# Optimization experiments

Hardware: AMD Instinct MI355X
Metric: run time of the kernel (lower is better)

Reference implementation:

```python
import jax, jax.numpy as jnp
import numpy as np
from jax import lax

B, C, D, H, W = 2, 256, 32, 64, 192
TRAIN_W = 640
DISPS = np.arange(D, dtype=np.float32) * 0.01  # norm_disp_range


def conv1x1(x, w, b):
    # x [B,Cin,H,W], w [Cout,Cin]
    return jnp.einsum('bchw,oc->bohw', x, w) + b[None, :, None, None]


def conv3x3(x, w, b):
    y = lax.conv_general_dilated(x, w, (1, 1), 'SAME',
                                 dimension_numbers=('NCHW', 'OIHW', 'NCHW'))
    return y + b[None, :, None, None]


def warp_volume(x, shift_px):
    """Horizontal bilinear warp with border clamp for each disparity.
    x [B,Cc,H,W], shift_px [B,D] (pixel shift) -> [B,Cc,D,H,W]."""
    Wd = x.shape[3]
    j = jnp.arange(Wd, dtype=x.dtype)
    src = jnp.clip(j[None, None, :] + shift_px[:, :, None], 0.0, Wd - 1.0)  # [B,D,W]
    x0 = jnp.floor(src).astype(jnp.int32)
    x1 = jnp.minimum(x0 + 1, Wd - 1)
    frac = src - x0.astype(src.dtype)  # [B,D,W]

    def one(xb, i0, i1, fb):
        g0 = xb[:, :, i0]  # [Cc,H,D,W]
        g1 = xb[:, :, i1]
        out = g0 * (1.0 - fb) + g1 * fb
        return out.transpose(0, 2, 1, 3)  # [Cc,D,H,W]

    return jax.vmap(one)(x, x0, x1, frac)


def setup_inputs() -> dict:
    key = jax.random.key(0)
    ks = jax.random.split(key, 16)
    f32 = jnp.float32
    inp = {
        't_feat': jax.random.normal(ks[0], (B, C, H, W), f32),
        's_feat': jax.random.normal(ks[1], (B, C, H, W), f32),
        'directs': jnp.ones((B, 1, 1, 1), f32),
        'qw': jax.random.normal(ks[2], (C // 4, C), f32) * 0.05,
        'qb': jax.random.normal(ks[3], (C // 4,), f32) * 0.05,
        'kw': jax.random.normal(ks[4], (C // 4, C), f32) * 0.05,
        'kb': jax.random.normal(ks[5], (C // 4,), f32) * 0.05,
        'vw': jax.random.normal(ks[6], (C // 4, C), f32) * 0.05,
        'vb': jax.random.normal(ks[7], (C // 4,), f32) * 0.05,
        'p1w': jax.random.normal(ks[8], (C // 4, C // 2, 3, 3), f32) * 0.05,
        'p1b': jax.random.normal(ks[9], (C // 4,), f32) * 0.05,
        'p2w': jax.random.normal(ks[10], (D, C // 4, 3, 3), f32) * 0.05,
        'p2b': jax.random.normal(ks[11], (D,), f32) * 0.05,
        'rw': jax.random.normal(ks[12], (C, C + D), f32) * 0.05,
        'rb': jax.random.normal(ks[13], (C,), f32) * 0.05,
        'img_w': TRAIN_W,
    }
    return inp


def reference(t_feat, s_feat, directs, qw, qb, kw, kb, vw, vb,
              p1w, p1b, p2w, p2b, rw, rb, img_w):
    rel_scale = (TRAIN_W / img_w) if img_w != TRAIN_W else 1.0
    q = conv1x1(t_feat, qw, qb)  # [B,C/4,H,W]
    k = conv1x1(s_feat, kw, kb)
    v = conv1x1(s_feat, vw, vb)

    Wd = t_feat.shape[3]
    disps = jnp.asarray(DISPS, t_feat.dtype)
    # normalized shift d*2*rel_scale*directs -> pixels: * (W-1)/2
    shift = disps[None, :] * rel_scale * directs.reshape(-1, 1) * (Wd - 1)  # [B,D]

    wk = warp_volume(k, shift)  # [B,C/4,D,H,W]
    wv = warp_volume(v, shift)

    cq = q.shape[1]
    cost = jnp.einsum('bchw,bcdhw->bdhw', q, wk) / (cq ** 0.5)  # [B,D,H,W]
    norm_cost = jax.nn.softmax(cost, axis=1)
    agg_v = jnp.einsum('bdhw,bcdhw->bchw', norm_cost, wv)  # [B,C/4,H,W]

    h1 = jax.nn.elu(conv3x3(jnp.concatenate([q, agg_v], axis=1), p1w, p1b))
    res_cost = conv3x3(h1, p2w, p2b)  # [B,D,H,W]
    cost = (cost + res_cost) * 0.5
    norm_cost = jax.nn.softmax(cost, axis=1)
    x = jax.nn.elu(conv1x1(jnp.concatenate([t_feat, norm_cost], axis=1), rw, rb))
    return x, cost
```

## Files before the change

kernel.cpp:

```cpp
#include <hip/hip_runtime.h>

#define BB 2
#define CC 256
#define CQ 64
#define DD 32
#define HH 64
#define WW 192
#define HW (HH*WW)
#define NPIX (BB*HW)

typedef __attribute__((ext_vector_type(8))) short bf16x8;
typedef __attribute__((ext_vector_type(4))) float f32x4;

__device__ __forceinline__ float b2f(ushort s){ return __uint_as_float(((uint)s)<<16); }
__device__ __forceinline__ ushort f2b(float f){
    uint u = __float_as_uint(f);
    return (ushort)((u + 0x7fffu + ((u>>16)&1u)) >> 16);
}
__device__ __forceinline__ float eluf(float v){ return v > 0.f ? v : (__expf(v)-1.f); }

__global__ __launch_bounds__(256) void k_prep_feat(
    const float* __restrict__ t_feat, const float* __restrict__ s_feat,
    ushort* __restrict__ Tt, ushort* __restrict__ Ts)
{
    __shared__ ushort sT[64*264];
    int blk = blockIdx.x;
    int which = blk / 384;
    int rem   = blk % 384;
    int b     = rem / 192;
    int tile  = rem % 192;
    int p0    = tile*64;
    const float* src = which ? s_feat : t_feat;
    ushort* dst      = which ? Ts : Tt;
    int tid = threadIdx.x;

    for (int i = tid; i < 2048; i += 256){
        int px  = i & 63;
        int c16 = i >> 6;
        const float* p = src + ((size_t)(b*CC + c16*8))*HW + p0 + px;
        uint u[4];
        #pragma unroll
        for (int j2=0;j2<4;++j2)
            u[j2] = (uint)f2b(p[(size_t)(2*j2)*HW]) | ((uint)f2b(p[(size_t)(2*j2+1)*HW])<<16);
        uint4 q4; q4.x=u[0]; q4.y=u[1]; q4.z=u[2]; q4.w=u[3];
        *(uint4*)&sT[(px*33 + c16)*8] = q4;
    }
    __syncthreads();
    for (int i = tid; i < 2048; i += 256){
        int c16 = i & 31;
        int px  = i >> 5;
        uint4 v = *(const uint4*)&sT[(px*33 + c16)*8];
        *(uint4*)(dst + ((size_t)(b*HW + p0 + px))*CC + c16*8) = v;
    }
}

__global__ __launch_bounds__(256) void k_prep_w(
    const float* __restrict__ qw, const float* __restrict__ qb,
    const float* __restrict__ kw, const float* __restrict__ kb,
    const float* __restrict__ vw, const float* __restrict__ vb,
    const float* __restrict__ p1w, const float* __restrict__ p2w,
    const float* __restrict__ rw,
    ushort* __restrict__ Wqkv, float* __restrict__ bqkv,
    ushort* __restrict__ A1, ushort* __restrict__ A2, ushort* __restrict__ Ar)
{
    int id = blockIdx.x*256 + threadIdx.x;
    if (id < 49152) {
        int o = id / 256, c = id % 256;
        float v = (o<64)? qw[o*256+c] : (o<128)? kw[(o-64)*256+c] : vw[(o-128)*256+c];
        Wqkv[id] = f2b(v);
    } else if (id < 49344) {
        int o = id - 49152;
        bqkv[o] = (o<64)? qb[o] : (o<128)? kb[o-64] : vb[o-128];
    } else if (id < 49344+73728) {
        int i = id - 49344;
        int o = i/1152, r = i%1152, t = r/128, ci = r%128;
        A1[i] = f2b(p1w[(size_t)(o*128+ci)*9 + t]);
    } else if (id < 49344+73728+18432) {
        int i = id - (49344+73728);
        int o = i/576, r = i%576, t = r/64, ci = r%64;
        A2[i] = f2b(p2w[(size_t)(o*64+ci)*9 + t]);
    } else if (id < 49344+73728+18432+73728) {
        int i = id - (49344+73728+18432);
        Ar[i] = f2b(rw[i]);
    }
}

__global__ __launch_bounds__(256) void g_qkv(
    const ushort* __restrict__ Tt, const ushort* __restrict__ Ts,
    const ushort* __restrict__ Wqkv, const float* __restrict__ bqkv,
    ushort* __restrict__ X1, ushort* __restrict__ VbT)
{
    __shared__ ushort sT[32*264];
    __shared__ ushort sS[32*264];
    int tid = threadIdx.x;
    int bid = blockIdx.x;
    int tile = (bid & 7)*96 + (bid >> 3);
    int p0 = tile * 32;

    for (int i = tid; i < 1024; i += 256){
        int px = i >> 5, c16 = i & 31;
        size_t gsrc = ((size_t)(p0 + px))*CC + c16*8;
        *(uint4*)&sT[(px*33 + c16)*8] = *(const uint4*)(Tt + gsrc);
        *(uint4*)&sS[(px*33 + c16)*8] = *(const uint4*)(Ts + gsrc);
    }
    __syncthreads();

    int wv = tid >> 6, lane = tid & 63;
    int lm = lane & 15, lk = lane >> 4;
    f32x4 acc[3][2];
    #pragma unroll
    for (int g=0;g<3;++g){ acc[g][0]=(f32x4){0.f,0.f,0.f,0.f}; acc[g][1]=(f32x4){0.f,0.f,0.f,0.f}; }
    const ushort* Ap = Wqkv + (size_t)(wv*16 + lm)*CC + lk*8;

    #pragma unroll
    for (int k0=0; k0<CC; k0+=32){
        bf16x8 a0 = *(const bf16x8*)(Ap + k0);
        bf16x8 a1 = *(const bf16x8*)(Ap + 64*CC + k0);
        bf16x8 a2 = *(const bf16x8*)(Ap + 128*CC + k0);
        #pragma unroll
        for (int nt=0; nt<2; ++nt){
            int ch = (nt*16+lm)*33 + (k0>>3) + lk;
            bf16x8 bT = *(const bf16x8*)&sT[ch*8];
            bf16x8 bS = *(const bf16x8*)&sS[ch*8];
            acc[0][nt] = __builtin_amdgcn_mfma_f32_16x16x32_bf16(a0, bT, acc[0][nt], 0,0,0);
            acc[1][nt] = __builtin_amdgcn_mfma_f32_16x16x32_bf16(a1, bS, acc[1][nt], 0,0,0);
            acc[2][nt] = __builtin_amdgcn_mfma_f32_16x16x32_bf16(a2, bS, acc[2][nt], 0,0,0);
        }
    }
    int ol = wv*16 + lk*4;
    #pragma unroll
    for (int nt=0; nt<2; ++nt){
        int p = p0 + nt*16 + lm;
        {
            int ob = ol;
            uint u0 = (uint)f2b(acc[0][nt][0]+bqkv[ob])   | ((uint)f2b(acc[0][nt][1]+bqkv[ob+1])<<16);
            uint u1 = (uint)f2b(acc[0][nt][2]+bqkv[ob+2]) | ((uint)f2b(acc[0][nt][3]+bqkv[ob+3])<<16);
            *(uint2*)(X1 + (size_t)p*128 + ol) = make_uint2(u0, u1);
        }
        {
            int ob = 64 + ol;
            uint u0 = (uint)f2b(acc[1][nt][0]+bqkv[ob])   | ((uint)f2b(acc[1][nt][1]+bqkv[ob+1])<<16);
            uint u1 = (uint)f2b(acc[1][nt][2]+bqkv[ob+2]) | ((uint)f2b(acc[1][nt][3]+bqkv[ob+3])<<16);
            *(uint2*)(X1 + (size_t)p*128 + 64 + ol) = make_uint2(u0, u1);
        }
        #pragma unroll
        for (int j=0;j<4;++j)
            VbT[(size_t)(ol+j)*NPIX + p] = f2b(acc[2][nt][j] + bqkv[128 + ol + j]);
    }
}

#define BAND 160
#define VTS 168
#define STS 36
#define PFS 164
__global__ __launch_bounds__(512) void k_ca(
    const ushort* __restrict__ X1, const ushort* __restrict__ VbT,
    const float* __restrict__ directs, const int* __restrict__ img_w_p,
    float* __restrict__ C1, ushort* __restrict__ Agg)
{
    __shared__ ushort sQ[32*64];
    __shared__ ushort sK[BAND*64];
    __shared__ ushort sVT[64*VTS];
    __shared__ float  sF[BAND*STS];
    __shared__ ushort sPC[32*VTS];
    int tid = threadIdx.x;
    int j   = blockIdx.x;
    int r8  = j & 7;
    int kk  = j >> 3;
    int sub = kk % 6;
    int rhi = kk / 6;
    int row = rhi*8 + r8;
    int b   = row >> 6;
    int h   = row & 63;
    int w0  = sub * 32;
    size_t rowbase = (size_t)b*HW + (size_t)h*WW;

    for (int i = tid; i < BAND*8; i += 512){
        int x = i >> 3, c8 = i & 7;
        int gx = w0 - 64 + x;
        uint4 kv = make_uint4(0,0,0,0);
        if (gx >= 0 && gx < WW)
            kv = *(const uint4*)(X1 + (rowbase+gx)*128 + 64 + c8*8);
        *(uint4*)&sK[(x*8 + (c8 ^ (x&7)))*8] = kv;
    }
    for (int i = tid; i < 64*20; i += 512){
        int c = i / 20, k2 = i % 20;
        int gx = w0 - 64 + k2*8;
        uint4 vv = make_uint4(0,0,0,0);
        if (gx >= 0 && gx < WW)
            vv = *(const uint4*)(VbT + (size_t)c*NPIX + rowbase + gx);
        *(uint4*)&sVT[c*VTS + k2*8] = vv;
    }
    if (tid < 256){
        int px = tid >> 3, c8 = tid & 7;
        uint4 qv = *(const uint4*)(X1 + (rowbase + w0 + px)*128 + c8*8);
        *(uint4*)&sQ[(px*8 + (c8 ^ (px&7)))*8] = qv;
    }
    __syncthreads();

    int w8 = tid >> 6, lane = tid & 63;
    int lm = lane & 15, lk = lane >> 4;

    {
        int mt = w8 & 1;
        int qrow = mt*16 + lm;
        for (int nt = (w8 >> 1); nt < 10; nt += 4){
            int xrow = nt*16 + lm;
            f32x4 acc = {0.f,0.f,0.f,0.f};
            #pragma unroll
            for (int kt=0; kt<2; ++kt){
                bf16x8 a = *(const bf16x8*)&sQ[(qrow*8 + ((kt*4+lk) ^ (qrow&7)))*8];
                bf16x8 bbf = *(const bf16x8*)&sK[(xrow*8 + ((kt*4+lk) ^ (xrow&7)))*8];
                acc = __builtin_amdgcn_mfma_f32_16x16x32_bf16(a, bbf, acc, 0,0,0);
            }
            *(f32x4*)&sF[xrow*STS + mt*16 + lk*4] = acc;
        }
    }
    __syncthreads();

    int px  = tid >> 4;
    int l16 = tid & 15;
    int w   = w0 + px;
    size_t n = rowbase + w;
    int imw = img_w_p[0];
    float rel = (imw != 640) ? (640.0f/(float)imw) : 1.0f;
    float sf = 0.01f * rel * directs[b] * 191.0f;
    float wf = (float)w;

    float cost[2]; int xi0[2], xi1[2]; float frk[2];
    #pragma unroll
    for (int t=0; t<2; ++t){
        int d = l16*2 + t;
        float srcx = fminf(fmaxf(wf + (float)d*sf, 0.f), 191.0f);
        int x0 = (int)floorf(srcx);
        int x1 = min(x0+1, WW-1);
        float fr = srcx - (float)x0;
        int i0 = x0 - w0 + 64;
        int i1 = x1 - w0 + 64;
        xi0[t] = i0; xi1[t] = i1; frk[t] = fr;
        float s0 = sF[i0*STS + px];
        float s1 = sF[i1*STS + px];
        cost[t] = (s0 + fr*(s1-s0)) * 0.125f;
    }
    *(float2*)(C1 + n*DD + l16*2) = make_float2(cost[0], cost[1]);
    float mm = fmaxf(cost[0], cost[1]);
    mm = fmaxf(mm, __shfl_xor(mm, 1));
    mm = fmaxf(mm, __shfl_xor(mm, 2));
    mm = fmaxf(mm, __shfl_xor(mm, 4));
    mm = fmaxf(mm, __shfl_xor(mm, 8));
    float e0 = __expf(cost[0]-mm), e1 = __expf(cost[1]-mm);
    float ss = e0 + e1;
    ss += __shfl_xor(ss, 1);
    ss += __shfl_xor(ss, 2);
    ss += __shfl_xor(ss, 4);
    ss += __shfl_xor(ss, 8);
    float inv = 1.f/ss;
    float p0 = e0*inv, p1 = e1*inv;
    __syncthreads();

    for (int i = tid; i < (32*PFS)/4; i += 512)
        *(f32x4*)&sF[i*4] = (f32x4){0.f,0.f,0.f,0.f};
    __syncthreads();

    {
        float w1a = p0*frk[0], w0a = p0 - w1a;
        float w1b = p1*frk[1], w0b = p1 - w1b;
        atomicAdd(&sF[px*PFS + xi0[0]], w0a);
        atomicAdd(&sF[px*PFS + xi1[0]], w1a);
        atomicAdd(&sF[px*PFS + xi0[1]], w0b);
        atomicAdd(&sF[px*PFS + xi1[1]], w1b);
    }
    __syncthreads();

    {
        int base = l16*10;
        #pragma unroll
        for (int q=0; q<5; ++q){
            float2 v2 = *(const float2*)&sF[px*PFS + base + q*2];
            *(uint*)&sPC[px*VTS + base + q*2] = (uint)f2b(v2.x) | ((uint)f2b(v2.y)<<16);
        }
    }
    __syncthreads();

    {
        int mi = w8 & 3;
        int ni = w8 >> 2;
        int c  = mi*16 + lm;
        int wr = ni*16 + lm;
        f32x4 acc = {0.f,0.f,0.f,0.f};
        #pragma unroll
        for (int kt=0; kt<5; ++kt){
            bf16x8 a   = *(const bf16x8*)&sVT[c*VTS + kt*32 + lk*8];
            bf16x8 bbf = *(const bf16x8*)&sPC[wr*VTS + kt*32 + lk*8];
            acc = __builtin_amdgcn_mfma_f32_16x16x32_bf16(a, bbf, acc, 0,0,0);
        }
        uint u0 = (uint)f2b(acc[0]) | ((uint)f2b(acc[1])<<16);
        uint u1 = (uint)f2b(acc[2]) | ((uint)f2b(acc[3])<<16);
        *(uint2*)(Agg + (rowbase + w0 + wr)*64 + mi*16 + lk*4) = make_uint2(u0, u1);
    }
}

__global__ __launch_bounds__(256) void g_conv1(
    const ushort* __restrict__ X1, const ushort* __restrict__ Agg,
    const ushort* __restrict__ A1, const float* __restrict__ p1b,
    ushort* __restrict__ X2)
{
    __shared__ ushort sB[3*16*34*8];
    int tid = threadIdx.x;
    int wv = tid >> 6, lane = tid & 63;
    int lm = lane & 15, lk = lane >> 4;
    int bid = blockIdx.x;
    int tile = (bid & 7)*96 + (bid >> 3);
    int n0 = tile * 32;
    int b  = n0 / HW;
    int pl = n0 % HW;
    int h  = pl / WW, w0 = pl % WW;

    for (int i = tid; i < 1632; i += 256){
        int dh = i / 544, rem2 = i % 544;
        int c16 = rem2 / 34, x = rem2 % 34;
        int hh = h + dh - 1, wx = w0 + x - 1;
        uint4 val = make_uint4(0,0,0,0);
        if (hh >= 0 && hh < HH && wx >= 0 && wx < WW){
            size_t pix = (size_t)b*HW + (size_t)hh*WW + wx;
            val = (c16 < 8) ? *(const uint4*)(X1 + pix*128 + c16*8)
                            : *(const uint4*)(Agg + pix*64 + (c16-8)*8);
        }
        *(uint4*)&sB[((dh*16 + c16)*34 + x)*8] = val;
    }
    __syncthreads();

    int mw = wv & 1, nw = wv >> 1;
    const ushort* Ap = A1 + (size_t)(mw*32 + lm)*1152 + lk*8;
    f32x4 acc0 = {0.f,0.f,0.f,0.f}, acc1 = {0.f,0.f,0.f,0.f};
    int xb = nw*16 + lm;
    #pragma unroll
    for (int t=0; t<9; ++t){
        int dh = t/3, dw = t%3;
        #pragma unroll
        for (int c0=0; c0<128; c0+=32){
            bf16x8 bb = *(const bf16x8*)&sB[((dh*16 + (c0>>3)+lk)*34 + xb + dw)*8];
            bf16x8 a0 = *(const bf16x8*)(Ap + t*128 + c0);
            bf16x8 a1 = *(const bf16x8*)(Ap + (size_t)16*1152 + t*128 + c0);
            acc0 = __builtin_amdgcn_mfma_f32_16x16x32_bf16(a0, bb, acc0, 0,0,0);
            acc1 = __builtin_amdgcn_mfma_f32_16x16x32_bf16(a1, bb, acc1, 0,0,0);
        }
    }
    int pg = n0 + nw*16 + lm;
    int o0 = mw*32 + lk*4;
    {
        uint u0 = (uint)f2b(eluf(acc0[0]+p1b[o0]))   | ((uint)f2b(eluf(acc0[1]+p1b[o0+1]))<<16);
        uint u1 = (uint)f2b(eluf(acc0[2]+p1b[o0+2])) | ((uint)f2b(eluf(acc0[3]+p1b[o0+3]))<<16);
        *(uint2*)(X2 + (size_t)pg*64 + o0) = make_uint2(u0, u1);
        int o1 = o0 + 16;
        uint u2 = (uint)f2b(eluf(acc1[0]+p1b[o1]))   | ((uint)f2b(eluf(acc1[1]+p1b[o1+1]))<<16);
        uint u3 = (uint)f2b(eluf(acc1[2]+p1b[o1+2])) | ((uint)f2b(eluf(acc1[3]+p1b[o1+3]))<<16);
        *(uint2*)(X2 + (size_t)pg*64 + o1) = make_uint2(u2, u3);
    }
}

__global__ __launch_bounds__(256) void g_conv2(
    const ushort* __restrict__ X2, const ushort* __restrict__ A2,
    const float* __restrict__ p2b, const float* __restrict__ C1,
    float* __restrict__ cost_out, ushort* __restrict__ NC)
{
    __shared__ ushort sB[3*8*34*8];
    __shared__ float  sO[32*36];
    int tid = threadIdx.x;
    int wv = tid >> 6, lane = tid & 63;
    int lm = lane & 15, lk = lane >> 4;
    int bid = blockIdx.x;
    int tile = (bid & 7)*96 + (bid >> 3);
    int n0 = tile * 32;
    int b  = n0 / HW;
    int pl = n0 % HW;
    int h  = pl / WW, w0 = pl % WW;

    for (int i = tid; i < 816; i += 256){
        int dh = i / 272, rem2 = i % 272;
        int c16 = rem2 / 34, x = rem2 % 34;
        int hh = h + dh - 1, wx = w0 + x - 1;
        uint4 val = make_uint4(0,0,0,0);
        if (hh >= 0 && hh < HH && wx >= 0 && wx < WW)
            val = *(const uint4*)(X2 + ((size_t)b*HW + (size_t)hh*WW + wx)*64 + c16*8);
        *(uint4*)&sB[((dh*8 + c16)*34 + x)*8] = val;
    }
    __syncthreads();

    int mw = wv & 1, nw = wv >> 1;
    const ushort* Ap = A2 + (size_t)(mw*16 + lm)*576 + lk*8;
    f32x4 acc = {0.f,0.f,0.f,0.f};
    int xb = nw*16 + lm;
    #pragma unroll
    for (int t=0; t<9; ++t){
        int dh = t/3, dw = t%3;
        #pragma unroll
        for (int c0=0; c0<64; c0+=32){
            bf16x8 bb = *(const bf16x8*)&sB[((dh*8 + (c0>>3)+lk)*34 + xb + dw)*8];
            bf16x8 a  = *(const bf16x8*)(Ap + t*64 + c0);
            acc = __builtin_amdgcn_mfma_f32_16x16x32_bf16(a, bb, acc, 0,0,0);
        }
    }
    int pg = n0 + nw*16 + lm;
    int pll = pg % HW;
    int o = mw*16 + lk*4;
    f32x4 cv = *(const f32x4*)(C1 + (size_t)pg*DD + o);
    f32x4 outv;
    #pragma unroll
    for (int j=0;j<4;++j){
        outv[j] = (cv[j] + acc[j] + p2b[o+j]) * 0.5f;
        cost_out[((size_t)(b*DD + o + j))*HW + pll] = outv[j];
    }
    *(f32x4*)&sO[(nw*16 + lm)*36 + o] = outv;
    __syncthreads();

    {
        int px = tid >> 3;
        int g  = tid & 7;
        f32x4 v = *(const f32x4*)&sO[px*36 + g*4];
        float m = fmaxf(fmaxf(v[0],v[1]), fmaxf(v[2],v[3]));
        m = fmaxf(m, __shfl_xor(m, 1));
        m = fmaxf(m, __shfl_xor(m, 2));
        m = fmaxf(m, __shfl_xor(m, 4));
        float e[4]; float s = 0.f;
        #pragma unroll
        for (int j=0;j<4;++j){ e[j] = __expf(v[j]-m); s += e[j]; }
        s += __shfl_xor(s, 1);
        s += __shfl_xor(s, 2);
        s += __shfl_xor(s, 4);
        float invs = 1.f/s;
        uint u0 = (uint)f2b(e[0]*invs) | ((uint)f2b(e[1]*invs)<<16);
        uint u1 = (uint)f2b(e[2]*invs) | ((uint)f2b(e[3]*invs)<<16);
        *(uint2*)(NC + (size_t)(n0 + px)*DD + g*4) = make_uint2(u0, u1);
    }
}

__global__ __launch_bounds__(256) void g_final(
    const ushort* __restrict__ Tt, const ushort* __restrict__ NC,
    const ushort* __restrict__ Ar, const float* __restrict__ rb,
    float* __restrict__ xout)
{
    __shared__ ushort sT[32*264];
    __shared__ ushort sN[32*40];
    int tid = threadIdx.x;
    int bid = blockIdx.x;
    int tile = (bid & 7)*96 + (bid >> 3);
    int p0 = tile * 32;

    for (int i = tid; i < 1024; i += 256){
        int px = i >> 5, c16 = i & 31;
        *(uint4*)&sT[(px*33 + c16)*8] = *(const uint4*)(Tt + ((size_t)(p0+px))*CC + c16*8);
    }
    if (tid < 128){
        int px = tid >> 2, c4 = tid & 3;
        *(uint4*)&sN[(px*5 + c4)*8] = *(const uint4*)(NC + ((size_t)(p0+px))*DD + c4*8);
    }
    __syncthreads();

    int wv = tid >> 6, lane = tid & 63;
    int lm = lane & 15, lk = lane >> 4;
    f32x4 acc[4][2];
    #pragma unroll
    for (int mi=0;mi<4;++mi){ acc[mi][0]=(f32x4){0.f,0.f,0.f,0.f}; acc[mi][1]=(f32x4){0.f,0.f,0.f,0.f}; }
    const ushort* Ap = Ar + (size_t)(wv*64 + lm)*288 + lk*8;

    #pragma unroll
    for (int k0=0; k0<288; k0+=32){
        bf16x8 a[4];
        #pragma unroll
        for (int mi=0;mi<4;++mi) a[mi] = *(const bf16x8*)(Ap + (size_t)mi*16*288 + k0);
        #pragma unroll
        for (int nt=0; nt<2; ++nt){
            int prow = nt*16 + lm;
            bf16x8 bb = (k0 < 256) ? *(const bf16x8*)&sT[(prow*33 + (k0>>3) + lk)*8]
                                   : *(const bf16x8*)&sN[(prow*5 + lk)*8];
            #pragma unroll
            for (int mi=0;mi<4;++mi)
                acc[mi][nt] = __builtin_amdgcn_mfma_f32_16x16x32_bf16(a[mi], bb, acc[mi][nt], 0,0,0);
        }
    }
    #pragma unroll
    for (int mi=0;mi<4;++mi){
        int o = wv*64 + mi*16 + lk*4;
        #pragma unroll
        for (int nt=0; nt<2; ++nt){
            int p = p0 + nt*16 + lm;
            int b = p / HW, pl = p % HW;
            #pragma unroll
            for (int j=0;j<4;++j)
                xout[((size_t)(b*CC + o + j))*HW + pl] = eluf(acc[mi][nt][j] + rb[o+j]);
        }
    }
}

extern "C" void kernel_launch(void* const* d_in, const int* in_sizes, int n_in,
                              void* d_out, int out_size, void* d_ws, size_t ws_size,
                              hipStream_t stream)
{
    const float* t_feat = (const float*)d_in[0];
    const float* s_feat = (const float*)d_in[1];
    const float* directs= (const float*)d_in[2];
    const float* qw = (const float*)d_in[3];
    const float* qb = (const float*)d_in[4];
    const float* kw = (const float*)d_in[5];
    const float* kb = (const float*)d_in[6];
    const float* vw = (const float*)d_in[7];
    const float* vb = (const float*)d_in[8];
    const float* p1w= (const float*)d_in[9];
    const float* p1b= (const float*)d_in[10];
    const float* p2w= (const float*)d_in[11];
    const float* p2b= (const float*)d_in[12];
    const float* rw = (const float*)d_in[13];
    const float* rb = (const float*)d_in[14];
    const int* img_w= (const int*)d_in[15];

    char* wsb = (char*)d_ws;
    ushort* Tt   = (ushort*)(wsb + 0);
    char*  tsreg = wsb + 12582912;
    ushort* Ts   = (ushort*)tsreg;
    ushort* X2   = (ushort*)tsreg;
    float*  C1   = (float*)(tsreg + 3145728);
    ushort* Agg  = (ushort*)(tsreg + 6291456);
    ushort* X1   = (ushort*)(wsb + 25165824);
    ushort* VbT  = (ushort*)(wsb + 31457280);
    ushort* NC   = (ushort*)(wsb + 31457280);
    ushort* Wqkv = (ushort*)(wsb + 34603008);
    float*  bqkv = (float*) (wsb + 34701312);
    ushort* A1   = (ushort*)(wsb + 34702336);
    ushort* A2   = (ushort*)(wsb + 34849792);
    ushort* Ar   = (ushort*)(wsb + 34886656);
    if (ws_size < 35034112) return;

    float* xout     = (float*)d_out;
    float* cost_out = xout + (size_t)BB*CC*HW;

    k_prep_feat<<<768, 256, 0, stream>>>(t_feat, s_feat, Tt, Ts);
    k_prep_w  <<<841,  256, 0, stream>>>(qw,qb,kw,kb,vw,vb,p1w,p2w,rw, Wqkv,bqkv,A1,A2,Ar);
    g_qkv     <<<768,  256, 0, stream>>>(Tt, Ts, Wqkv, bqkv, X1, VbT);
    k_ca      <<<768,  512, 0, stream>>>(X1, VbT, directs, img_w, C1, Agg);
    g_conv1   <<<768,  256, 0, stream>>>(X1, Agg, A1, p1b, X2);
    g_conv2   <<<768,  256, 0, stream>>>(X2, A2, p2b, C1, cost_out, NC);
    g_final   <<<768,  256, 0, stream>>>(Tt, NC, Ar, rb, xout);
}
```

Baseline: 110.2 us.

## Merge prep kernels, fuse conv2 with final projection, load k_ca operands directly

Combines the feature and weight preparation kernels into one launch, and fuses the second 3x3 conv and its softmax with the final 1x1 projection so the normalized cost stays in shared memory. This removes the NC workspace round trip and two launches. In the cost-attention kernel, the Q/K/V shared-memory staging is replaced by direct global loads into MFMA operands, which cuts LDS use and barriers but adds redundant, less coalesced global reads. The fused kernel runs two GEMM phases per block and may hold more registers.

```diff
diff --git a/kernel.cpp b/kernel.cpp
--- a/kernel.cpp
+++ b/kernel.cpp
@@ -19,42 +19,9 @@
 }
 __device__ __forceinline__ float eluf(float v){ return v > 0.f ? v : (__expf(v)-1.f); }
 
-__global__ __launch_bounds__(256) void k_prep_feat(
+__global__ __launch_bounds__(256) void k_prep(
     const float* __restrict__ t_feat, const float* __restrict__ s_feat,
-    ushort* __restrict__ Tt, ushort* __restrict__ Ts)
-{
-    __shared__ ushort sT[64*264];
-    int blk = blockIdx.x;
-    int which = blk / 384;
-    int rem   = blk % 384;
-    int b     = rem / 192;
-    int tile  = rem % 192;
-    int p0    = tile*64;
-    const float* src = which ? s_feat : t_feat;
-    ushort* dst      = which ? Ts : Tt;
-    int tid = threadIdx.x;
-
-    for (int i = tid; i < 2048; i += 256){
-        int px  = i & 63;
-        int c16 = i >> 6;
-        const float* p = src + ((size_t)(b*CC + c16*8))*HW + p0 + px;
-        uint u[4];
-        #pragma unroll
-        for (int j2=0;j2<4;++j2)
-            u[j2] = (uint)f2b(p[(size_t)(2*j2)*HW]) | ((uint)f2b(p[(size_t)(2*j2+1)*HW])<<16);
-        uint4 q4; q4.x=u[0]; q4.y=u[1]; q4.z=u[2]; q4.w=u[3];
-        *(uint4*)&sT[(px*33 + c16)*8] = q4;
-    }
-    __syncthreads();
-    for (int i = tid; i < 2048; i += 256){
-        int c16 = i & 31;
-        int px  = i >> 5;
-        uint4 v = *(const uint4*)&sT[(px*33 + c16)*8];
-        *(uint4*)(dst + ((size_t)(b*HW + p0 + px))*CC + c16*8) = v;
-    }
-}
-
-__global__ __launch_bounds__(256) void k_prep_w(
+    ushort* __restrict__ Tt, ushort* __restrict__ Ts,
     const float* __restrict__ qw, const float* __restrict__ qb,
     const float* __restrict__ kw, const float* __restrict__ kb,
     const float* __restrict__ vw, const float* __restrict__ vb,
@@ -63,25 +30,57 @@
     ushort* __restrict__ Wqkv, float* __restrict__ bqkv,
     ushort* __restrict__ A1, ushort* __restrict__ A2, ushort* __restrict__ Ar)
 {
-    int id = blockIdx.x*256 + threadIdx.x;
-    if (id < 49152) {
-        int o = id / 256, c = id % 256;
-        float v = (o<64)? qw[o*256+c] : (o<128)? kw[(o-64)*256+c] : vw[(o-128)*256+c];
-        Wqkv[id] = f2b(v);
-    } else if (id < 49344) {
-        int o = id - 49152;
-        bqkv[o] = (o<64)? qb[o] : (o<128)? kb[o-64] : vb[o-128];
-    } else if (id < 49344+73728) {
-        int i = id - 49344;
-        int o = i/1152, r = i%1152, t = r/128, ci = r%128;
-        A1[i] = f2b(p1w[(size_t)(o*128+ci)*9 + t]);
-    } else if (id < 49344+73728+18432) {
-        int i = id - (49344+73728);
-        int o = i/576, r = i%576, t = r/64, ci = r%64;
-        A2[i] = f2b(p2w[(size_t)(o*64+ci)*9 + t]);
-    } else if (id < 49344+73728+18432+73728) {
-        int i = id - (49344+73728+18432);
-        Ar[i] = f2b(rw[i]);
+    __shared__ ushort sT[64*264];
+    int blk = blockIdx.x;
+    int tid = threadIdx.x;
+    if (blk >= 768){
+        int id = (blk - 768)*256 + tid;
+        if (id < 49152) {
+            int o = id / 256, c = id % 256;
+            float v = (o<64)? qw[o*256+c] : (o<128)? kw[(o-64)*256+c] : vw[(o-128)*256+c];
+            Wqkv[id] = f2b(v);
+        } else if (id < 49344) {
+            int o = id - 49152;
+            bqkv[o] = (o<64)? qb[o] : (o<128)? kb[o-64] : vb[o-128];
+        } else if (id < 49344+73728) {
+            int i = id - 49344;
+            int o = i/1152, r = i%1152, t = r/128, ci = r%128;
+            A1[i] = f2b(p1w[(size_t)(o*128+ci)*9 + t]);
+        } else if (id < 49344+73728+18432) {
+            int i = id - (49344+73728);
+            int o = i/576, r = i%576, t = r/64, ci = r%64;
+            A2[i] = f2b(p2w[(size_t)(o*64+ci)*9 + t]);
+        } else if (id < 49344+73728+18432+73728) {
+            int i = id - (49344+73728+18432);
+            Ar[i] = f2b(rw[i]);
+        }
+        return;
+    }
+    int which = blk / 384;
+    int rem   = blk % 384;
+    int b     = rem / 192;
+    int tile  = rem % 192;
+    int p0    = tile*64;
+    const float* src = which ? s_feat : t_feat;
+    ushort* dst      = which ? Ts : Tt;
+
+    for (int i = tid; i < 2048; i += 256){
+        int px  = i & 63;
+        int c16 = i >> 6;
+        const float* p = src + ((size_t)(b*CC + c16*8))*HW + p0 + px;
+        uint u[4];
+        #pragma unroll
+        for (int j2=0;j2<4;++j2)
+            u[j2] = (uint)f2b(p[(size_t)(2*j2)*HW]) | ((uint)f2b(p[(size_t)(2*j2+1)*HW])<<16);
+        uint4 q4; q4.x=u[0]; q4.y=u[1]; q4.z=u[2]; q4.w=u[3];
+        *(uint4*)&sT[(px*33 + c16)*8] = q4;
+    }
+    __syncthreads();
+    for (int i = tid; i < 2048; i += 256){
+        int c16 = i & 31;
+        int px  = i >> 5;
+        uint4 v = *(const uint4*)&sT[(px*33 + c16)*8];
+        *(uint4*)(dst + ((size_t)(b*HW + p0 + px))*CC + c16*8) = v;
     }
 }
 
@@ -150,17 +149,14 @@
 }
 
 #define BAND 160
-#define VTS 168
 #define STS 36
 #define PFS 164
+#define VTS 168
 __global__ __launch_bounds__(512) void k_ca(
     const ushort* __restrict__ X1, const ushort* __restrict__ VbT,
     const float* __restrict__ directs, const int* __restrict__ img_w_p,
     float* __restrict__ C1, ushort* __restrict__ Agg)
 {
-    __shared__ ushort sQ[32*64];
-    __shared__ ushort sK[BAND*64];
-    __shared__ ushort sVT[64*VTS];
     __shared__ float  sF[BAND*STS];
     __shared__ ushort sPC[32*VTS];
     int tid = threadIdx.x;
@@ -175,44 +171,27 @@
     int w0  = sub * 32;
     size_t rowbase = (size_t)b*HW + (size_t)h*WW;
 
-    for (int i = tid; i < BAND*8; i += 512){
-        int x = i >> 3, c8 = i & 7;
-        int gx = w0 - 64 + x;
-        uint4 kv = make_uint4(0,0,0,0);
-        if (gx >= 0 && gx < WW)
-            kv = *(const uint4*)(X1 + (rowbase+gx)*128 + 64 + c8*8);
-        *(uint4*)&sK[(x*8 + (c8 ^ (x&7)))*8] = kv;
-    }
-    for (int i = tid; i < 64*20; i += 512){
-        int c = i / 20, k2 = i % 20;
-        int gx = w0 - 64 + k2*8;
-        uint4 vv = make_uint4(0,0,0,0);
-        if (gx >= 0 && gx < WW)
-            vv = *(const uint4*)(VbT + (size_t)c*NPIX + rowbase + gx);
-        *(uint4*)&sVT[c*VTS + k2*8] = vv;
-    }
-    if (tid < 256){
-        int px = tid >> 3, c8 = tid & 7;
-        uint4 qv = *(const uint4*)(X1 + (rowbase + w0 + px)*128 + c8*8);
-        *(uint4*)&sQ[(px*8 + (c8 ^ (px&7)))*8] = qv;
-    }
-    __syncthreads();
-
     int w8 = tid >> 6, lane = tid & 63;
     int lm = lane & 15, lk = lane >> 4;
 
     {
         int mt = w8 & 1;
-        int qrow = mt*16 + lm;
+        int q  = w0 + mt*16 + lm;
+        const ushort* Qp = X1 + (rowbase + q)*128 + lk*8;
+        bf16x8 aq0 = *(const bf16x8*)(Qp);
+        bf16x8 aq1 = *(const bf16x8*)(Qp + 32);
         for (int nt = (w8 >> 1); nt < 10; nt += 4){
             int xrow = nt*16 + lm;
+            int gx = w0 - 64 + xrow;
+            bf16x8 b0 = {0,0,0,0,0,0,0,0}, b1 = {0,0,0,0,0,0,0,0};
+            if (gx >= 0 && gx < WW){
+                const ushort* Kp = X1 + (rowbase + gx)*128 + 64 + lk*8;
+                b0 = *(const bf16x8*)(Kp);
+                b1 = *(const bf16x8*)(Kp + 32);
+            }
             f32x4 acc = {0.f,0.f,0.f,0.f};
-            #pragma unroll
-            for (int kt=0; kt<2; ++kt){
-                bf16x8 a = *(const bf16x8*)&sQ[(qrow*8 + ((kt*4+lk) ^ (qrow&7)))*8];
-                bf16x8 bbf = *(const bf16x8*)&sK[(xrow*8 + ((kt*4+lk) ^ (xrow&7)))*8];
-                acc = __builtin_amdgcn_mfma_f32_16x16x32_bf16(a, bbf, acc, 0,0,0);
-            }
+            acc = __builtin_amdgcn_mfma_f32_16x16x32_bf16(aq0, b0, acc, 0,0,0);
+            acc = __builtin_amdgcn_mfma_f32_16x16x32_bf16(aq1, b1, acc, 0,0,0);
             *(f32x4*)&sF[xrow*STS + mt*16 + lk*4] = acc;
         }
     }
@@ -287,10 +266,13 @@
         int ni = w8 >> 2;
         int c  = mi*16 + lm;
         int wr = ni*16 + lm;
+        const ushort* Vp = VbT + (size_t)c*NPIX + rowbase + w0 - 64;
         f32x4 acc = {0.f,0.f,0.f,0.f};
         #pragma unroll
         for (int kt=0; kt<5; ++kt){
-            bf16x8 a   = *(const bf16x8*)&sVT[c*VTS + kt*32 + lk*8];
+            int gx = w0 - 64 + kt*32 + lk*8;
+            bf16x8 a = {0,0,0,0,0,0,0,0};
+            if (gx >= 0 && gx < WW) a = *(const bf16x8*)(Vp + kt*32 + lk*8);
             bf16x8 bbf = *(const bf16x8*)&sPC[wr*VTS + kt*32 + lk*8];
             acc = __builtin_amdgcn_mfma_f32_16x16x32_bf16(a, bbf, acc, 0,0,0);
         }
@@ -359,13 +341,17 @@
     }
 }
 
-__global__ __launch_bounds__(256) void g_conv2(
+__global__ __launch_bounds__(256) void g_conv2final(
     const ushort* __restrict__ X2, const ushort* __restrict__ A2,
     const float* __restrict__ p2b, const float* __restrict__ C1,
-    float* __restrict__ cost_out, ushort* __restrict__ NC)
+    const ushort* __restrict__ Tt, const ushort* __restrict__ Ar,
+    const float* __restrict__ rb,
+    float* __restrict__ cost_out, float* __restrict__ xout)
 {
-    __shared__ ushort sB[3*8*34*8];
+    __shared__ ushort sT[32*264];
     __shared__ float  sO[32*36];
+    __shared__ ushort sN[32*40];
+    ushort* sB = sT;
     int tid = threadIdx.x;
     int wv = tid >> 6, lane = tid & 63;
     int lm = lane & 15, lk = lane >> 4;
@@ -387,31 +373,33 @@
     }
     __syncthreads();
 
-    int mw = wv & 1, nw = wv >> 1;
-    const ushort* Ap = A2 + (size_t)(mw*16 + lm)*576 + lk*8;
-    f32x4 acc = {0.f,0.f,0.f,0.f};
-    int xb = nw*16 + lm;
-    #pragma unroll
-    for (int t=0; t<9; ++t){
-        int dh = t/3, dw = t%3;
-        #pragma unroll
-        for (int c0=0; c0<64; c0+=32){
-            bf16x8 bb = *(const bf16x8*)&sB[((dh*8 + (c0>>3)+lk)*34 + xb + dw)*8];
-            bf16x8 a  = *(const bf16x8*)(Ap + t*64 + c0);
-            acc = __builtin_amdgcn_mfma_f32_16x16x32_bf16(a, bb, acc, 0,0,0);
-        }
-    }
-    int pg = n0 + nw*16 + lm;
-    int pll = pg % HW;
-    int o = mw*16 + lk*4;
-    f32x4 cv = *(const f32x4*)(C1 + (size_t)pg*DD + o);
-    f32x4 outv;
-    #pragma unroll
-    for (int j=0;j<4;++j){
-        outv[j] = (cv[j] + acc[j] + p2b[o+j]) * 0.5f;
-        cost_out[((size_t)(b*DD + o + j))*HW + pll] = outv[j];
-    }
-    *(f32x4*)&sO[(nw*16 + lm)*36 + o] = outv;
+    {
+        int mw = wv & 1, nw = wv >> 1;
+        const ushort* Ap = A2 + (size_t)(mw*16 + lm)*576 + lk*8;
+        f32x4 acc = {0.f,0.f,0.f,0.f};
+        int xb = nw*16 + lm;
+        #pragma unroll
+        for (int t=0; t<9; ++t){
+            int dh = t/3, dw = t%3;
+            #pragma unroll
+            for (int c0=0; c0<64; c0+=32){
+                bf16x8 bb = *(const bf16x8*)&sB[((dh*8 + (c0>>3)+lk)*34 + xb + dw)*8];
+                bf16x8 a  = *(const bf16x8*)(Ap + t*64 + c0);
+                acc = __builtin_amdgcn_mfma_f32_16x16x32_bf16(a, bb, acc, 0,0,0);
+            }
+        }
+        int pg = n0 + nw*16 + lm;
+        int pll = pg % HW;
+        int o = mw*16 + lk*4;
+        f32x4 cv = *(const f32x4*)(C1 + (size_t)pg*DD + o);
+        f32x4 outv;
+        #pragma unroll
+        for (int j=0;j<4;++j){
+            outv[j] = (cv[j] + acc[j] + p2b[o+j]) * 0.5f;
+            cost_out[((size_t)(b*DD + o + j))*HW + pll] = outv[j];
+        }
+        *(f32x4*)&sO[(nw*16 + lm)*36 + o] = outv;
+    }
     __syncthreads();
 
     {
@@ -431,64 +419,46 @@
         float invs = 1.f/s;
         uint u0 = (uint)f2b(e[0]*invs) | ((uint)f2b(e[1]*invs)<<16);
         uint u1 = (uint)f2b(e[2]*invs) | ((uint)f2b(e[3]*invs)<<16);
-        *(uint2*)(NC + (size_t)(n0 + px)*DD + g*4) = make_uint2(u0, u1);
-    }
-}
-
-__global__ __launch_bounds__(256) void g_final(
-    const ushort* __restrict__ Tt, const ushort* __restrict__ NC,
-    const ushort* __restrict__ Ar, const float* __restrict__ rb,
-    float* __restrict__ xout)
-{
-    __shared__ ushort sT[32*264];
-    __shared__ ushort sN[32*40];
-    int tid = threadIdx.x;
-    int bid = blockIdx.x;
-    int tile = (bid & 7)*96 + (bid >> 3);
-    int p0 = tile * 32;
-
+        *(uint2*)&sN[px*40 + g*4] = make_uint2(u0, u1);
+    }
     for (int i = tid; i < 1024; i += 256){
         int px = i >> 5, c16 = i & 31;
-        *(uint4*)&sT[(px*33 + c16)*8] = *(const uint4*)(Tt + ((size_t)(p0+px))*CC + c16*8);
-    }
-    if (tid < 128){
-        int px = tid >> 2, c4 = tid & 3;
-        *(uint4*)&sN[(px*5 + c4)*8] = *(const uint4*)(NC + ((size_t)(p0+px))*DD + c4*8);
-    }
-    __syncthreads();
-
-    int wv = tid >> 6, lane = tid & 63;
-    int lm = lane & 15, lk = lane >> 4;
-    f32x4 acc[4][2];
-    #pragma unroll
-    for (int mi=0;mi<4;++mi){ acc[mi][0]=(f32x4){0.f,0.f,0.f,0.f}; acc[mi][1]=(f32x4){0.f,0.f,0.f,0.f}; }
-    const ushort* Ap = Ar + (size_t)(wv*64 + lm)*288 + lk*8;
-
-    #pragma unroll
-    for (int k0=0; k0<288; k0+=32){
-        bf16x8 a[4];
-        #pragma unroll
-        for (int mi=0;mi<4;++mi) a[mi] = *(const bf16x8*)(Ap + (size_t)mi*16*288 + k0);
-        #pragma unroll
-        for (int nt=0; nt<2; ++nt){
-            int prow = nt*16 + lm;
-            bf16x8 bb = (k0 < 256) ? *(const bf16x8*)&sT[(prow*33 + (k0>>3) + lk)*8]
-                                   : *(const bf16x8*)&sN[(prow*5 + lk)*8];
+        *(uint4*)&sT[(px*33 + c16)*8] = *(const uint4*)(Tt + ((size_t)(n0+px))*CC + c16*8);
+    }
+    __syncthreads();
+
+    {
+        f32x4 acc[4][2];
+        #pragma unroll
+        for (int mi=0;mi<4;++mi){ acc[mi][0]=(f32x4){0.f,0.f,0.f,0.f}; acc[mi][1]=(f32x4){0.f,0.f,0.f,0.f}; }
+        const ushort* Ap = Ar + (size_t)(wv*64 + lm)*288 + lk*8;
+
+        #pragma unroll
+        for (int k0=0; k0<288; k0+=32){
+            bf16x8 a[4];
             #pragma unroll
-            for (int mi=0;mi<4;++mi)
-                acc[mi][nt] = __builtin_amdgcn_mfma_f32_16x16x32_bf16(a[mi], bb, acc[mi][nt], 0,0,0);
-        }
-    }
-    #pragma unroll
-    for (int mi=0;mi<4;++mi){
-        int o = wv*64 + mi*16 + lk*4;
-        #pragma unroll
-        for (int nt=0; nt<2; ++nt){
-            int p = p0 + nt*16 + lm;
-            int b = p / HW, pl = p % HW;
+            for (int mi=0;mi<4;++mi) a[mi] = *(const bf16x8*)(Ap + (size_t)mi*16*288 + k0);
             #pragma unroll
-            for (int j=0;j<4;++j)
-                xout[((size_t)(b*CC + o + j))*HW + pl] = eluf(acc[mi][nt][j] + rb[o+j]);
+            for (int nt=0; nt<2; ++nt){
+                int prow = nt*16 + lm;
+                bf16x8 bb = (k0 < 256) ? *(const bf16x8*)&sT[(prow*33 + (k0>>3) + lk)*8]
+                                       : *(const bf16x8*)&sN[(prow*5 + lk)*8];
+                #pragma unroll
+                for (int mi=0;mi<4;++mi)
+                    acc[mi][nt] = __builtin_amdgcn_mfma_f32_16x16x32_bf16(a[mi], bb, acc[mi][nt], 0,0,0);
+            }
+        }
+        #pragma unroll
+        for (int mi=0;mi<4;++mi){
+            int o = wv*64 + mi*16 + lk*4;
+            #pragma unroll
+            for (int nt=0; nt<2; ++nt){
+                int p = n0 + nt*16 + lm;
+                int bb2 = p / HW, pl2 = p % HW;
+                #pragma unroll
+                for (int j=0;j<4;++j)
+                    xout[((size_t)(bb2*CC + o + j))*HW + pl2] = eluf(acc[mi][nt][j] + rb[o+j]);
+            }
         }
     }
 }
@@ -523,7 +493,6 @@
     ushort* Agg  = (ushort*)(tsreg + 6291456);
     ushort* X1   = (ushort*)(wsb + 25165824);
     ushort* VbT  = (ushort*)(wsb + 31457280);
-    ushort* NC   = (ushort*)(wsb + 31457280);
     ushort* Wqkv = (ushort*)(wsb + 34603008);
     float*  bqkv = (float*) (wsb + 34701312);
     ushort* A1   = (ushort*)(wsb + 34702336);
@@ -534,11 +503,12 @@
     float* xout     = (float*)d_out;
     float* cost_out = xout + (size_t)BB*CC*HW;
 
-    k_prep_feat<<<768, 256, 0, stream>>>(t_feat, s_feat, Tt, Ts);
-    k_prep_w  <<<841,  256, 0, stream>>>(qw,qb,kw,kb,vw,vb,p1w,p2w,rw, Wqkv,bqkv,A1,A2,Ar);
-    g_qkv     <<<768,  256, 0, stream>>>(Tt, Ts, Wqkv, bqkv, X1, VbT);
-    k_ca      <<<768,  512, 0, stream>>>(X1, VbT, directs, img_w, C1, Agg);
-    g_conv1   <<<768,  256, 0, stream>>>(X1, Agg, A1, p1b, X2);
-    g_conv2   <<<768,  256, 0, stream>>>(X2, A2, p2b, C1, cost_out, NC);
-    g_final   <<<768,  256, 0, stream>>>(Tt, NC, Ar, rb, xout);
-}
+    k_prep      <<<1609, 256, 0, stream>>>(t_feat, s_feat, Tt, Ts,
+                                           qw,qb,kw,kb,vw,vb,p1w,p2w,rw,
+                                           Wqkv,bqkv,A1,A2,Ar);
+    g_qkv       <<<768,  256, 0, stream>>>(Tt, Ts, Wqkv, bqkv, X1, VbT);
+    k_ca        <<<768,  512, 0, stream>>>(X1, VbT, directs, img_w, C1, Agg);
+    g_conv1     <<<768,  256, 0, stream>>>(X1, Agg, A1, p1b, X2);
+    g_conv2final<<<768,  256, 0, stream>>>(X2, A2, p2b, C1, Tt, Ar, rb,
+                                           cost_out, xout);
+}
```

Result: faster. 104.0 us (-5.6%).
